# Optimization experiments

Measured on AMD Instinct MI355X. Metric: run time of the kernel, lower is better.

## Reference

```python
import math
import jax, jax.numpy as jnp
import numpy as np

N_HEAD = 16
N_EMBD = 1024
HEAD_DIM = N_EMBD // N_HEAD  # 64
SHARED = 16
PRIV = HEAD_DIM - SHARED     # 48
B, T = 4, 2048
STD = 0.02


def setup_inputs() -> dict:
    key = jax.random.key(0)
    ks = jax.random.split(key, 6)
    x = jax.random.normal(ks[0], (B, T, N_EMBD), dtype=jnp.float32)
    # Linear params stored as (in, out); bias zeros per _reset_parameters
    W_share = jax.random.normal(ks[1], (N_EMBD, SHARED), dtype=jnp.float32) * STD
    Wq = jax.random.normal(ks[2], (N_EMBD, N_HEAD * PRIV), dtype=jnp.float32) * STD
    Wk = jax.random.normal(ks[3], (N_EMBD, N_HEAD * PRIV), dtype=jnp.float32) * STD
    Wv = jax.random.normal(ks[4], (N_EMBD, N_EMBD), dtype=jnp.float32) * STD
    Wo = jax.random.normal(ks[5], (N_EMBD, N_EMBD), dtype=jnp.float32) * STD
    return {
        'hidden_states': x,
        'W_share': W_share, 'b_share': jnp.zeros((SHARED,), jnp.float32),
        'Wq': Wq, 'bq': jnp.zeros((N_HEAD * PRIV,), jnp.float32),
        'Wk': Wk, 'bk': jnp.zeros((N_HEAD * PRIV,), jnp.float32),
        'Wv': Wv, 'bv': jnp.zeros((N_EMBD,), jnp.float32),
        'Wo': Wo, 'bo': jnp.zeros((N_EMBD,), jnp.float32),
    }


def reference(hidden_states, W_share, b_share, Wq, bq, Wk, bk, Wv, bv, Wo, bo):
    x = hidden_states
    Bt, Tt, C = x.shape
    # shared projection, broadcast across heads: (B,T,s) -> (B,H,T,s)
    share = x @ W_share + b_share
    share_h = jnp.broadcast_to(share[:, None, :, :], (Bt, N_HEAD, Tt, SHARED))
    # private q/k: (B,T,H*p) -> (B,H,T,p)
    q_priv = (x @ Wq + bq).reshape(Bt, Tt, N_HEAD, PRIV).transpose(0, 2, 1, 3)
    k_priv = (x @ Wk + bk).reshape(Bt, Tt, N_HEAD, PRIV).transpose(0, 2, 1, 3)
    q = jnp.concatenate([share_h, q_priv], axis=-1)  # (B,H,T,head_dim)
    k = jnp.concatenate([share_h, k_priv], axis=-1)
    v = (x @ Wv + bv).reshape(Bt, Tt, N_HEAD, HEAD_DIM).transpose(0, 2, 1, 3)
    scale = 1.0 / math.sqrt(HEAD_DIM)
    att = jnp.einsum('bhqd,bhkd->bhqk', q, k) * scale
    causal = jnp.tril(jnp.ones((Tt, Tt), dtype=bool))
    att = jnp.where(causal[None, None, :, :], att, -jnp.inf)
    att = jax.nn.softmax(att, axis=-1)
    y = jnp.einsum('bhqk,bhkd->bhqd', att, v)
    y = y.transpose(0, 2, 1, 3).reshape(Bt, Tt, C)
    y = y @ Wo + bo
    return y
```

## Files before the change

kernel.cpp:

```cpp
#include <hip/hip_runtime.h>
#include <hip/hip_bf16.h>

typedef unsigned short u16;
typedef short short8 __attribute__((ext_vector_type(8)));
typedef float f32x4 __attribute__((ext_vector_type(4)));

#define N_EMBD   1024
#define N_HEADS  16
#define HEAD_DIM 64
#define PRIV     48
#define SEQ_T    2048
#define BATCH    4
#define M_ROWS   (BATCH*SEQ_T)
#define PNS      2816
#define NTILES   (SEQ_T/64)
#define NT_K     16

#if __has_builtin(__builtin_amdgcn_exp2f)
#define EXP2(x) __builtin_amdgcn_exp2f(x)
#else
#define EXP2(x) exp2f(x)
#endif

#if __has_builtin(__builtin_amdgcn_global_load_lds)
#define HAVE_GLL 1
#else
#define HAVE_GLL 0
#endif

__device__ __forceinline__ u16 f2bf(float f) {
  __hip_bfloat16 h = __float2bfloat16(f);
  return *reinterpret_cast<u16*>(&h);
}
__device__ __forceinline__ float bf2f(u16 s) {
  __hip_bfloat16 h;
  *reinterpret_cast<u16*>(&h) = s;
  return __bfloat162float(h);
}
__device__ __forceinline__ float loadv(const void* p, size_t i, int isf32) {
  return isf32 ? ((const float*)p)[i] : bf2f(((const u16*)p)[i]);
}
__device__ __forceinline__ u16 truncbf(float f) {
  unsigned u = __builtin_bit_cast(unsigned, f);
  return (u16)(u >> 16);
}
#if HAVE_GLL
__device__ __forceinline__ void gload_lds16(const u16* g, u16* l) {
  __builtin_amdgcn_global_load_lds(
      (const __attribute__((address_space(1))) void*)g,
      (__attribute__((address_space(3))) void*)l, 16, 0, 0);
}
#endif

__global__ __launch_bounds__(256) void detect_kernel(const u16* __restrict__ x,
                                                     int* __restrict__ flag) {
  __shared__ int cnt;
  if (threadIdx.x == 0) cnt = 0;
  __syncthreads();
  u16 v = x[2 * threadIdx.x];
  int e = (v >> 7) & 0xFF;
  int junk = (e >= 0xC0 || (e != 0 && e <= 0x30)) ? 1 : 0;
  if (junk) atomicAdd(&cnt, 1);
  __syncthreads();
  if (threadIdx.x == 0) *flag = (cnt > 16) ? 1 : 0;
}

__global__ __launch_bounds__(256) void pack_t_kernel(
    const void* __restrict__ Wsh, const void* __restrict__ Wq,
    const void* __restrict__ Wk,  const void* __restrict__ Wv,
    const void* __restrict__ Wo,
    const void* __restrict__ bsh, const void* __restrict__ bq,
    const void* __restrict__ bk,  const void* __restrict__ bv,
    const void* __restrict__ bo,
    u16* __restrict__ Wcat, u16* __restrict__ Woc,
    u16* __restrict__ bcat, u16* __restrict__ boc,
    const int* __restrict__ flagp)
{
  const int f = *flagp;
  if (blockIdx.z == 5) {
    const int flat = blockIdx.y * 16 + blockIdx.x;
    const int padN = (PNS - 2576) * 1024;
    for (int i = flat * 256 + threadIdx.x; i < padN; i += 256 * 256)
      Wcat[(size_t)2576 * 1024 + i] = 0;
    if (flat == 0) {
      for (int c = threadIdx.x; c < PNS; c += 256) {
        float v = 0.f;
        if (c < 16)        v = loadv(bsh, c, f);
        else if (c < 784)  v = loadv(bq, c - 16, f);
        else if (c < 1552) v = loadv(bk, c - 784, f);
        else if (c < 2576) v = loadv(bv, c - 1552, f);
        bcat[c] = f2bf(v);
      }
    } else if (flat == 1) {
      for (int c = threadIdx.x; c < N_EMBD; c += 256)
        boc[c] = f2bf(loadv(bo, c, f));
    }
    return;
  }
  const void* src; u16* dst; int N, rowOff;
  switch (blockIdx.z) {
    case 0: src = Wsh; dst = Wcat; N = 16;   rowOff = 0;    break;
    case 1: src = Wq;  dst = Wcat; N = 768;  rowOff = 16;   break;
    case 2: src = Wk;  dst = Wcat; N = 768;  rowOff = 784;  break;
    case 3: src = Wv;  dst = Wcat; N = 1024; rowOff = 1552; break;
    default:src = Wo;  dst = Woc;  N = 1024; rowOff = 0;    break;
  }
  const int n0 = blockIdx.x * 64;
  if (n0 >= N) return;
  const int k0 = blockIdx.y * 64;
  __shared__ u16 t[64][65];
  const int tx = threadIdx.x & 63, ty = threadIdx.x >> 6;
#pragma unroll
  for (int rr = 0; rr < 16; rr++) {
    int k = k0 + ty * 16 + rr;
    int n = n0 + tx;
    float v = (n < N) ? loadv(src, (size_t)k * N + n, f) : 0.f;
    t[ty * 16 + rr][tx] = f2bf(v);
  }
  __syncthreads();
#pragma unroll
  for (int rr = 0; rr < 16; rr++) {
    int n = ty * 16 + rr;
    if (n0 + n < N)
      dst[(size_t)(rowOff + n0 + n) * 1024 + k0 + tx] = t[tx][n];
  }
}

__global__ __launch_bounds__(256) void xbf_kernel(const void* __restrict__ x,
                                                  u16* __restrict__ Xb,
                                                  const int* __restrict__ flagp) {
  const int f = *flagp;
  const size_t i = (size_t)blockIdx.x * 256 + threadIdx.x;
  if (f) {
    const float4* p = (const float4*)x;
    float4 a = p[i * 2], b = p[i * 2 + 1];
    u16 t[8] = {f2bf(a.x), f2bf(a.y), f2bf(a.z), f2bf(a.w),
                f2bf(b.x), f2bf(b.y), f2bf(b.z), f2bf(b.w)};
    *(uint4*)&Xb[i * 8] = *(const uint4*)t;
  } else {
    *(uint4*)&Xb[i * 8] = ((const uint4*)x)[i];
  }
}

__global__ __launch_bounds__(512, 2) void gemm8p_kernel(
    const u16* __restrict__ A,
    const u16* __restrict__ Bt,
    const u16* __restrict__ bias,
    void* __restrict__ C, int ldc, int Mtiles,
    const int* __restrict__ flagp, int c_dyn)
{
  __shared__ __align__(16) u16 smem[73728];
  u16* const As = smem;
  u16* const Bs = smem + 3 * 8192;

  const bool cf32 = (c_dyn != 0) && (*flagp != 0);

  const int tid  = threadIdx.x;
  const int lane = tid & 63;
  const int w    = tid >> 6;
  const int quad = lane >> 4, l16 = lane & 15;
  const int wm   = w >> 2, wn = w & 3;

  const int nwg = gridDim.x;
  const int wg  = (blockIdx.x & 7) * (nwg >> 3) + (blockIdx.x >> 3);
  const int mb  = wg % Mtiles, nb = wg / Mtiles;
  const int m0  = mb * 128, n0 = nb * 256;

  int ldsA[2]; size_t glA[2];
  int ldsB[2][2]; size_t glB[2][2];
#pragma unroll
  for (int rd = 0; rd < 2; rd++) {
    int j = tid + rd * 512, rp = j >> 3, s = j & 7;
    int cl = (s ^ (rp & 7)) * 8;
    ldsA[rd] = rp * 64 + s * 8;
    glA[rd]  = (size_t)(m0 + rp) * 1024 + cl;
#pragma unroll
    for (int nh = 0; nh < 2; nh++) {
      int cc = (rp & 31) + nh * 32 + (rp >> 5) * 64;
      ldsB[nh][rd] = cc * 64 + s * 8;
      glB[nh][rd]  = (size_t)(n0 + cc) * 1024 + cl;
    }
  }

#if HAVE_GLL
#define G8(g, l) gload_lds16((g), (l))
#else
#define G8(g, l) (*(uint4*)(l) = *(const uint4*)(g))
#endif
#define STG_A(t, bf)                                                       \
  if ((t) < NT_K) {                                                        \
    _Pragma("unroll") for (int rd = 0; rd < 2; rd++)                       \
      G8(A + glA[rd] + (t) * 64, As + (bf) * 8192 + ldsA[rd]);             \
  }
#define STG_B(nh, t, bf)                                                   \
  if ((t) < NT_K) {                                                        \
    _Pragma("unroll") for (int rd = 0; rd < 2; rd++)                       \
      G8(Bt + glB[nh][rd] + (t) * 64, Bs + (bf) * 16384 + ldsB[nh][rd]);   \
  }

  const int ck0  = ((quad)     ^ (l16 & 7)) * 8;
  const int ck1  = ((4 + quad) ^ (l16 & 7)) * 8;
  const int arow = (wm * 64 + l16) * 64;
  const int brow = (wn * 64 + l16) * 64;

  f32x4 acc[4][4];
#pragma unroll
  for (int i = 0; i < 4; i++)
#pragma unroll
    for (int j = 0; j < 4; j++) acc[i][j] = (f32x4){0.f, 0.f, 0.f, 0.f};

  short8 af[4][2], bA[2][2], bB[2][2];

#define READ_A(cur)                                                        \
  { const u16* pa = As + (cur) * 8192 + arow;                              \
    _Pragma("unroll") for (int m = 0; m < 4; m++) {                        \
      af[m][0] = *(const short8*)(pa + m * 1024 + ck0);                    \
      af[m][1] = *(const short8*)(pa + m * 1024 + ck1); } }
#define READ_B(dst, nh, cur)                                               \
  { const u16* pb = Bs + (cur) * 16384 + brow + (nh) * 2048;               \
    _Pragma("unroll") for (int n = 0; n < 2; n++) {                        \
      dst[n][0] = *(const short8*)(pb + n * 1024 + ck0);                   \
      dst[n][1] = *(const short8*)(pb + n * 1024 + ck1); } }
#define MM16(bfr, nh)                                                      \
  __builtin_amdgcn_s_setprio(1);                                           \
  _Pragma("unroll") for (int m = 0; m < 4; m++)                            \
    _Pragma("unroll") for (int n = 0; n < 2; n++) {                        \
      acc[m][(nh)*2+n] = __builtin_amdgcn_mfma_f32_16x16x32_bf16(          \
          af[m][0], bfr[n][0], acc[m][(nh)*2+n], 0, 0, 0);                 \
      acc[m][(nh)*2+n] = __builtin_amdgcn_mfma_f32_16x16x32_bf16(          \
          af[m][1], bfr[n][1], acc[m][(nh)*2+n], 0, 0, 0); }               \
  __builtin_amdgcn_s_setprio(0);
#define BARR { __builtin_amdgcn_s_barrier(); __builtin_amdgcn_sched_barrier(0); }

  STG_A(0, 0); STG_B(1, 0, 0); STG_B(0, 0, 0);
  STG_A(1, 1); STG_B(1, 1, 1); STG_B(0, 1, 1);
  asm volatile("s_waitcnt vmcnt(6)");
  BARR;

#pragma unroll
  for (int kt = 0; kt < NT_K; kt++) {
    const int cur = kt % 3;
    const int stb = (kt + 2) % 3;
    READ_A(cur); READ_B(bA, 0, cur);
    STG_A(kt + 2, stb); STG_B(1, kt + 2, stb);
    BARR;
    MM16(bA, 0);
    BARR;
    READ_B(bB, 1, cur);
    STG_B(0, kt + 2, stb);
    BARR;
    MM16(bB, 1);
    if (kt < NT_K - 2)       { asm volatile("s_waitcnt vmcnt(6)"); }
    else if (kt == NT_K - 2) { asm volatile("s_waitcnt vmcnt(0)"); }
    BARR;
  }
#undef STG_A
#undef STG_B
#undef READ_A
#undef READ_B
#undef MM16
#undef BARR
#undef G8

  float bvv[4];
#pragma unroll
  for (int ni = 0; ni < 4; ni++)
    bvv[ni] = bf2f(bias[n0 + wn * 64 + ni * 16 + l16]);

  if (!cf32) {
    u16* cs = smem + w * 4096;
#pragma unroll
    for (int m = 0; m < 4; m++)
#pragma unroll
      for (int ni = 0; ni < 4; ni++)
#pragma unroll
        for (int r = 0; r < 4; r++) {
          int row = m * 16 + quad * 4 + r;
          int ch  = ((ni * 2 + (l16 >> 3)) ^ (row & 7)) * 8 + (l16 & 7);
          cs[row * 64 + ch] = f2bf(acc[m][ni][r] + bvv[ni]);
        }
    u16* Cb = (u16*)C;
#pragma unroll
    for (int i = 0; i < 8; i++) {
      int ch = lane + i * 64;
      int rr = ch >> 3, cc = ch & 7;
      short8 v = *(const short8*)(cs + rr * 64 + ((cc ^ (rr & 7)) * 8));
      *(short8*)&Cb[(size_t)(m0 + wm * 64 + rr) * ldc + n0 + wn * 64 + cc * 8] = v;
    }
  } else {
    float* cf = (float*)(void*)smem + w * 2048;
#pragma unroll
    for (int pass = 0; pass < 2; pass++) {
#pragma unroll
      for (int m2 = 0; m2 < 2; m2++)
#pragma unroll
        for (int ni = 0; ni < 4; ni++)
#pragma unroll
          for (int r = 0; r < 4; r++) {
            int row = m2 * 16 + quad * 4 + r;
            int ch  = ((ni * 4 + (l16 >> 2)) ^ (row & 15)) * 4 + (l16 & 3);
            cf[row * 64 + ch] = acc[pass * 2 + m2][ni][r] + bvv[ni];
          }
      float* Cf = (float*)C;
#pragma unroll
      for (int i = 0; i < 8; i++) {
        int ch = lane + i * 64;
        int rr = ch >> 4, cc = ch & 15;
        f32x4 v = *(const f32x4*)(cf + rr * 64 + ((cc ^ (rr & 15)) * 4));
        *(f32x4*)&Cf[(size_t)(m0 + wm * 64 + pass * 32 + rr) * ldc +
                     n0 + wn * 64 + cc * 4] = v;
      }
    }
  }
}

__global__ __launch_bounds__(256) void vt_kernel(const u16* __restrict__ P,
                                                 u16* __restrict__ Vt)
{
  const int tt = blockIdx.x * 64;
  const int bh = blockIdx.y;
  const int b = bh >> 4, h = bh & 15;
  const int vcol = 1552 + h * HEAD_DIM;
  __shared__ u16 t[64][65];
  const int tx = threadIdx.x & 63, ty = threadIdx.x >> 6;
#pragma unroll
  for (int rr = 0; rr < 16; rr++) {
    int r = ty * 16 + rr;
    t[r][tx] = P[((size_t)b * SEQ_T + tt + r) * PNS + vcol + tx];
  }
  __syncthreads();
#pragma unroll
  for (int rr = 0; rr < 16; rr++) {
    int d = ty * 16 + rr;
    Vt[((size_t)bh * 64 + d) * SEQ_T + tt + tx] = t[tx][d];
  }
}

__global__ __launch_bounds__(256, 2) void attn_kernel(
    const u16* __restrict__ P, const u16* __restrict__ Vt,
    u16* __restrict__ Y)
{
  const int bh  = blockIdx.x;
  const int b   = bh >> 4, h = bh & 15;
  const int p   = blockIdx.y;
  const int qtA = p, qtB = NTILES - 1 - p;
  const int tid = threadIdx.x;
  const int w   = tid >> 6;
  const int lane = tid & 63;
  const int quad = lane >> 4, l16 = lane & 15;
  const size_t rowb = (size_t)b * SEQ_T;
  const int qcol = 16 + h * PRIV;
  const int kcol = 784 + h * PRIV;

  __shared__ __align__(16) u16 Ks[3][64 * 64];
  __shared__ __align__(16) u16 Vs[3][64 * 64];
  __shared__ __align__(16) u16 Ps[4][2][16 * 68];

  const float csc = 0.18033688011112042f;
  const int d0  = quad * 8;
  const int cq0 = (d0 < 16) ? d0 : (qcol + d0 - 16);
  const int iA = qtA * 64 + w * 16, iB = qtB * 64 + w * 16;
  const u16* qrowA = P + (rowb + iA + l16) * PNS;
  const u16* qrowB = P + (rowb + iB + l16) * PNS;
  short8 qaA0 = *(const short8*)&qrowA[cq0];
  short8 qaA1 = *(const short8*)&qrowA[qcol + 16 + d0];
  short8 qaB0 = *(const short8*)&qrowB[cq0];
  short8 qaB1 = *(const short8*)&qrowB[qcol + 16 + d0];
#pragma unroll
  for (int e = 0; e < 8; e++) {
    qaA0[e] = (short)f2bf(bf2f((u16)qaA0[e]) * csc);
    qaA1[e] = (short)f2bf(bf2f((u16)qaA1[e]) * csc);
    qaB0[e] = (short)f2bf(bf2f((u16)qaB0[e]) * csc);
    qaB1[e] = (short)f2bf(bf2f((u16)qaB1[e]) * csc);
  }
  short8 ones;
#pragma unroll
  for (int e = 0; e < 8; e++) ones[e] = (short)0x3F80;

  const int nkt = qtB + 1;

#if HAVE_GLL
#define GLOADA(g, l) gload_lds16((g), (l))
#else
#define GLOADA(g, l) (*(uint4*)(l) = *(const uint4*)(g))
#endif
#define STAGE_KV(t, bb)                                                        \
  {                                                                            \
    const int kk0 = (t) * 64;                                                  \
    _Pragma("unroll") for (int i2 = 0; i2 < 2; i2++) {                         \
      int c   = tid + i2 * 256;                                                \
      int row = c >> 3;                                                        \
      int dg  = ((c & 7) ^ (row & 7)) * 8;                                     \
      int col = (dg < 16) ? dg : (kcol + dg - 16);                             \
      GLOADA(&P[(rowb + kk0 + row) * PNS + col], &Ks[bb][c * 8]);              \
      GLOADA(&Vt[((size_t)bh * 64 + row) * SEQ_T + kk0 + dg], &Vs[bb][c * 8]); \
    }                                                                          \
  }

  f32x4 accyA[4], accyB[4], acclA, acclB;
#pragma unroll
  for (int g = 0; g < 4; g++) {
    accyA[g] = (f32x4){0.f, 0.f, 0.f, 0.f};
    accyB[g] = (f32x4){0.f, 0.f, 0.f, 0.f};
  }
  acclA = (f32x4){0.f, 0.f, 0.f, 0.f};
  acclB = (f32x4){0.f, 0.f, 0.f, 0.f};

  STAGE_KV(0, 0);
  STAGE_KV(1, 1);
  asm volatile("s_waitcnt vmcnt(4)" ::: "memory");
  __builtin_amdgcn_sched_barrier(0);
  __builtin_amdgcn_s_barrier();

  for (int kt = 0; kt < nkt; kt++) {
    const int cur = kt % 3;
    const int k0  = kt * 64;
    if (kt + 2 < nkt) STAGE_KV(kt + 2, (kt + 2) % 3);

    const bool doA = (kt <= qtA);

    float svA[4][4], svB[4][4];
    __builtin_amdgcn_s_setprio(1);
#pragma unroll
    for (int g = 0; g < 4; g++) {
      int j = g * 16 + l16;
      short8 kb0 = *(const short8*)&Ks[cur][j * 64 + ((quad    ) ^ (j & 7)) * 8];
      short8 kb1 = *(const short8*)&Ks[cur][j * 64 + ((quad + 4) ^ (j & 7)) * 8];
      f32x4 sB = (f32x4){0.f, 0.f, 0.f, 0.f};
      sB = __builtin_amdgcn_mfma_f32_16x16x32_bf16(qaB0, kb0, sB, 0, 0, 0);
      sB = __builtin_amdgcn_mfma_f32_16x16x32_bf16(qaB1, kb1, sB, 0, 0, 0);
#pragma unroll
      for (int r = 0; r < 4; r++) svB[g][r] = sB[r];
      if (doA) {
        f32x4 sA = (f32x4){0.f, 0.f, 0.f, 0.f};
        sA = __builtin_amdgcn_mfma_f32_16x16x32_bf16(qaA0, kb0, sA, 0, 0, 0);
        sA = __builtin_amdgcn_mfma_f32_16x16x32_bf16(qaA1, kb1, sA, 0, 0, 0);
#pragma unroll
        for (int r = 0; r < 4; r++) svA[g][r] = sA[r];
      }
    }
    __builtin_amdgcn_s_setprio(0);
    if (kt == qtA && doA) {
#pragma unroll
      for (int g = 0; g < 4; g++)
#pragma unroll
        for (int r = 0; r < 4; r++) {
          int gi = iA + quad * 4 + r;
          int gj = k0 + g * 16 + l16;
          if (gj > gi) svA[g][r] = -__builtin_inff();
        }
    }
    if (kt == qtB) {
#pragma unroll
      for (int g = 0; g < 4; g++)
#pragma unroll
        for (int r = 0; r < 4; r++) {
          int gi = iB + quad * 4 + r;
          int gj = k0 + g * 16 + l16;
          if (gj > gi) svB[g][r] = -__builtin_inff();
        }
    }

    if (doA) {
#pragma unroll
      for (int g = 0; g < 4; g++)
#pragma unroll
        for (int r = 0; r < 4; r++)
          Ps[w][0][(quad * 4 + r) * 68 + g * 16 + l16] = truncbf(EXP2(svA[g][r]));
    }
#pragma unroll
    for (int g = 0; g < 4; g++)
#pragma unroll
      for (int r = 0; r < 4; r++)
        Ps[w][1][(quad * 4 + r) * 68 + g * 16 + l16] = truncbf(EXP2(svB[g][r]));

    __builtin_amdgcn_s_setprio(1);
#pragma unroll
    for (int kf = 0; kf < 2; kf++) {
      short8 vb[4];
#pragma unroll
      for (int g2 = 0; g2 < 4; g2++) {
        int row = g2 * 16 + l16;
        vb[g2] = *(const short8*)&Vs[cur][row * 64 + (((kf * 4 + quad) ^ (row & 7)) * 8)];
      }
      short8 paB = *(const short8*)&Ps[w][1][l16 * 68 + kf * 32 + quad * 8];
      acclB = __builtin_amdgcn_mfma_f32_16x16x32_bf16(paB, ones, acclB, 0, 0, 0);
#pragma unroll
      for (int g2 = 0; g2 < 4; g2++)
        accyB[g2] = __builtin_amdgcn_mfma_f32_16x16x32_bf16(paB, vb[g2], accyB[g2], 0, 0, 0);
      if (doA) {
        short8 paA = *(const short8*)&Ps[w][0][l16 * 68 + kf * 32 + quad * 8];
        acclA = __builtin_amdgcn_mfma_f32_16x16x32_bf16(paA, ones, acclA, 0, 0, 0);
#pragma unroll
        for (int g2 = 0; g2 < 4; g2++)
          accyA[g2] = __builtin_amdgcn_mfma_f32_16x16x32_bf16(paA, vb[g2], accyA[g2], 0, 0, 0);
      }
    }
    __builtin_amdgcn_s_setprio(0);

    if (kt + 3 < nkt) {
      asm volatile("s_waitcnt vmcnt(4)" ::: "memory");
      __builtin_amdgcn_sched_barrier(0);
      __builtin_amdgcn_s_barrier();
    } else if (kt + 2 == nkt) {
      asm volatile("s_waitcnt vmcnt(0)" ::: "memory");
      __builtin_amdgcn_sched_barrier(0);
      __builtin_amdgcn_s_barrier();
    } else if (kt + 3 == nkt) {
      asm volatile("s_waitcnt vmcnt(4)" ::: "memory");
      __builtin_amdgcn_sched_barrier(0);
      __builtin_amdgcn_s_barrier();
    }
  }
#undef STAGE_KV
#undef GLOADA

  float invA[4], invB[4];
#pragma unroll
  for (int r = 0; r < 4; r++) {
    invA[r] = 1.0f / acclA[r];
    invB[r] = 1.0f / acclB[r];
  }
#pragma unroll
  for (int g2 = 0; g2 < 4; g2++) {
    int col = h * HEAD_DIM + g2 * 16 + l16;
#pragma unroll
    for (int r = 0; r < 4; r++) {
      int giA = iA + quad * 4 + r;
      int giB = iB + quad * 4 + r;
      Y[(rowb + giA) * N_EMBD + col] = f2bf(accyA[g2][r] * invA[r]);
      Y[(rowb + giB) * N_EMBD + col] = f2bf(accyB[g2][r] * invB[r]);
    }
  }
}

extern "C" void kernel_launch(void* const* d_in, const int* in_sizes, int n_in,
                              void* d_out, int out_size, void* d_ws, size_t ws_size,
                              hipStream_t stream) {
  (void)in_sizes; (void)n_in; (void)out_size; (void)ws_size;
  const void* x   = d_in[0];
  const void* Wsh = d_in[1];
  const void* bsh = d_in[2];
  const void* Wq  = d_in[3];
  const void* bq  = d_in[4];
  const void* Wk  = d_in[5];
  const void* bk  = d_in[6];
  const void* Wv  = d_in[7];
  const void* bv  = d_in[8];
  const void* Wo  = d_in[9];
  const void* bo  = d_in[10];

  char* wsb = (char*)d_ws;
  int* flag = (int*)wsb;
  u16* ws16 = (u16*)(wsb + 64);
  u16* Wcat = ws16;
  u16* bcat = Wcat + (size_t)PNS * N_EMBD;
  u16* Woc  = bcat + PNS;
  u16* boc  = Woc + (size_t)N_EMBD * N_EMBD;
  u16* Pb   = boc + N_EMBD;
  u16* Yb   = Pb + (size_t)M_ROWS * PNS;
  u16* Vtb  = Yb + (size_t)M_ROWS * N_EMBD;
  u16* Xb   = Yb;

  detect_kernel<<<dim3(1), dim3(256), 0, stream>>>((const u16*)x, flag);
  pack_t_kernel<<<dim3(16, 16, 6), dim3(256), 0, stream>>>(
      Wsh, Wq, Wk, Wv, Wo, bsh, bq, bk, bv, bo, Wcat, Woc, bcat, boc, flag);
  xbf_kernel<<<dim3(M_ROWS * N_EMBD / (256 * 8)), dim3(256), 0, stream>>>(
      x, Xb, flag);
  gemm8p_kernel<<<dim3(64 * (PNS / 256)), dim3(512), 0, stream>>>(
      Xb, Wcat, bcat, Pb, PNS, 64, flag, 0);
  vt_kernel<<<dim3(SEQ_T / 64, BATCH * N_HEADS), dim3(256), 0, stream>>>(
      Pb, Vtb);
  attn_kernel<<<dim3(BATCH * N_HEADS, NTILES / 2), dim3(256), 0, stream>>>(
      Pb, Vtb, Yb);
  gemm8p_kernel<<<dim3(64 * (N_EMBD / 256)), dim3(512), 0, stream>>>(
      Yb, Woc, boc, d_out, N_EMBD, 64, flag, 1);
}
```

Baseline: 284.0 us.

## Switch attention to 32x32 MFMA with register-resident P via lane shuffles

Rewrites the attention inner loop to use 32x32x16 MFMA tiles that cover both the A and B query blocks in one 32-row tile, computing S transposed so that P stays in registers. P is packed to bf16 with v_cvt_pk and exchanged across half-waves with shuffles instead of going through LDS. The per-warp P shared buffer is removed and launch bounds are raised to 3 blocks per CU. The tradeoff is that A rows are computed even when masked (kt > qtA), which wastes MFMA work on those blocks, and the change adds shuffle cost and register pressure.

```diff
diff --git a/kernel.cpp b/kernel.cpp
--- a/kernel.cpp
+++ b/kernel.cpp
@@ -4,6 +4,8 @@
 typedef unsigned short u16;
 typedef short short8 __attribute__((ext_vector_type(8)));
 typedef float f32x4 __attribute__((ext_vector_type(4)));
+typedef float f32x16 __attribute__((ext_vector_type(16)));
+typedef unsigned uint32x4 __attribute__((ext_vector_type(4)));
 
 #define N_EMBD   1024
 #define N_HEADS  16
@@ -336,7 +338,7 @@
   }
 }
 
-__global__ __launch_bounds__(256, 2) void attn_kernel(
+__global__ __launch_bounds__(256, 3) void attn_kernel(
     const u16* __restrict__ P, const u16* __restrict__ Vt,
     u16* __restrict__ Y)
 {
@@ -347,32 +349,30 @@
   const int tid = threadIdx.x;
   const int w   = tid >> 6;
   const int lane = tid & 63;
-  const int quad = lane >> 4, l16 = lane & 15;
+  const int l32 = lane & 31, hi = lane >> 5;
   const size_t rowb = (size_t)b * SEQ_T;
   const int qcol = 16 + h * PRIV;
   const int kcol = 784 + h * PRIV;
 
   __shared__ __align__(16) u16 Ks[3][64 * 64];
   __shared__ __align__(16) u16 Vs[3][64 * 64];
-  __shared__ __align__(16) u16 Ps[4][2][16 * 68];
 
   const float csc = 0.18033688011112042f;
-  const int d0  = quad * 8;
-  const int cq0 = (d0 < 16) ? d0 : (qcol + d0 - 16);
   const int iA = qtA * 64 + w * 16, iB = qtB * 64 + w * 16;
-  const u16* qrowA = P + (rowb + iA + l16) * PNS;
-  const u16* qrowB = P + (rowb + iB + l16) * PNS;
-  short8 qaA0 = *(const short8*)&qrowA[cq0];
-  short8 qaA1 = *(const short8*)&qrowA[qcol + 16 + d0];
-  short8 qaB0 = *(const short8*)&qrowB[cq0];
-  short8 qaB1 = *(const short8*)&qrowB[qcol + 16 + d0];
-#pragma unroll
-  for (int e = 0; e < 8; e++) {
-    qaA0[e] = (short)f2bf(bf2f((u16)qaA0[e]) * csc);
-    qaA1[e] = (short)f2bf(bf2f((u16)qaA1[e]) * csc);
-    qaB0[e] = (short)f2bf(bf2f((u16)qaB0[e]) * csc);
-    qaB1[e] = (short)f2bf(bf2f((u16)qaB1[e]) * csc);
-  }
+  const int gi = (l32 < 16) ? (iA + l32) : (iB + l32 - 16);
+  const u16* qptr = P + (rowb + gi) * PNS;
+
+  short8 qb[4];
+  qb[0] = *(const short8*)&qptr[8 * hi];
+#pragma unroll
+  for (int c = 1; c < 4; c++)
+    qb[c] = *(const short8*)&qptr[qcol + 16 * c + 8 * hi - 16];
+#pragma unroll
+  for (int c = 0; c < 4; c++)
+#pragma unroll
+    for (int e = 0; e < 8; e++)
+      qb[c][e] = (short)f2bf(bf2f((u16)qb[c][e]) * csc);
+
   short8 ones;
 #pragma unroll
   for (int e = 0; e < 8; e++) ones[e] = (short)0x3F80;
@@ -397,14 +397,11 @@
     }                                                                          \
   }
 
-  f32x4 accyA[4], accyB[4], acclA, acclB;
-#pragma unroll
-  for (int g = 0; g < 4; g++) {
-    accyA[g] = (f32x4){0.f, 0.f, 0.f, 0.f};
-    accyB[g] = (f32x4){0.f, 0.f, 0.f, 0.f};
-  }
-  acclA = (f32x4){0.f, 0.f, 0.f, 0.f};
-  acclB = (f32x4){0.f, 0.f, 0.f, 0.f};
+  f32x16 accy[2], accl;
+#pragma unroll
+  for (int r = 0; r < 16; r++) { accy[0][r] = 0.f; accy[1][r] = 0.f; accl[r] = 0.f; }
+
+  const float ninf = -__builtin_inff();
 
   STAGE_KV(0, 0);
   STAGE_KV(1, 1);
@@ -417,86 +414,66 @@
     const int k0  = kt * 64;
     if (kt + 2 < nkt) STAGE_KV(kt + 2, (kt + 2) % 3);
 
-    const bool doA = (kt <= qtA);
-
-    float svA[4][4], svB[4][4];
-    __builtin_amdgcn_s_setprio(1);
-#pragma unroll
-    for (int g = 0; g < 4; g++) {
-      int j = g * 16 + l16;
-      short8 kb0 = *(const short8*)&Ks[cur][j * 64 + ((quad    ) ^ (j & 7)) * 8];
-      short8 kb1 = *(const short8*)&Ks[cur][j * 64 + ((quad + 4) ^ (j & 7)) * 8];
-      f32x4 sB = (f32x4){0.f, 0.f, 0.f, 0.f};
-      sB = __builtin_amdgcn_mfma_f32_16x16x32_bf16(qaB0, kb0, sB, 0, 0, 0);
-      sB = __builtin_amdgcn_mfma_f32_16x16x32_bf16(qaB1, kb1, sB, 0, 0, 0);
-#pragma unroll
-      for (int r = 0; r < 4; r++) svB[g][r] = sB[r];
-      if (doA) {
-        f32x4 sA = (f32x4){0.f, 0.f, 0.f, 0.f};
-        sA = __builtin_amdgcn_mfma_f32_16x16x32_bf16(qaA0, kb0, sA, 0, 0, 0);
-        sA = __builtin_amdgcn_mfma_f32_16x16x32_bf16(qaA1, kb1, sA, 0, 0, 0);
-#pragma unroll
-        for (int r = 0; r < 4; r++) svA[g][r] = sA[r];
+#pragma unroll
+    for (int kk = 0; kk < 2; kk++) {
+      f32x16 s;
+#pragma unroll
+      for (int r = 0; r < 16; r++) s[r] = 0.f;
+      const int krow = kk * 32 + l32;
+      __builtin_amdgcn_s_setprio(1);
+#pragma unroll
+      for (int c = 0; c < 4; c++) {
+        short8 ka = *(const short8*)&Ks[cur][krow * 64 + (((2 * c + hi) ^ (krow & 7)) * 8)];
+        s = __builtin_amdgcn_mfma_f32_32x32x16_bf16(ka, qb[c], s, 0, 0, 0);
+      }
+      __builtin_amdgcn_s_setprio(0);
+
+      if (kt == qtA || kt == qtB) {
+#pragma unroll
+        for (int r = 0; r < 16; r++) {
+          int gj = k0 + kk * 32 + (r & 3) + 8 * (r >> 2) + 4 * hi;
+          if (gj > gi) s[r] = ninf;
+        }
+      }
+      if (kt > qtA) {
+#pragma unroll
+        for (int r = 0; r < 16; r++)
+          if (l32 < 16) s[r] = ninf;
+      }
+
+      float px[16];
+#pragma unroll
+      for (int r = 0; r < 16; r++) px[r] = EXP2(s[r]);
+
+#pragma unroll
+      for (int kc = 0; kc < 2; kc++) {
+        unsigned g0, g1, g2, g3;
+        asm("v_cvt_pk_bf16_f32 %0, %1, %2" : "=v"(g0) : "v"(px[8*kc+0]), "v"(px[8*kc+1]));
+        asm("v_cvt_pk_bf16_f32 %0, %1, %2" : "=v"(g1) : "v"(px[8*kc+2]), "v"(px[8*kc+3]));
+        asm("v_cvt_pk_bf16_f32 %0, %1, %2" : "=v"(g2) : "v"(px[8*kc+4]), "v"(px[8*kc+5]));
+        asm("v_cvt_pk_bf16_f32 %0, %1, %2" : "=v"(g3) : "v"(px[8*kc+6]), "v"(px[8*kc+7]));
+        unsigned x0 = (unsigned)__shfl_xor((int)g0, 32);
+        unsigned x1 = (unsigned)__shfl_xor((int)g1, 32);
+        unsigned x2 = (unsigned)__shfl_xor((int)g2, 32);
+        unsigned x3 = (unsigned)__shfl_xor((int)g3, 32);
+        unsigned v0 = hi ? x2 : g0;
+        unsigned v1 = hi ? x3 : g1;
+        unsigned v2 = hi ? g2 : x0;
+        unsigned v3 = hi ? g3 : x1;
+        uint32x4 pv = {v0, v1, v2, v3};
+        short8 pa = __builtin_bit_cast(short8, pv);
+
+        __builtin_amdgcn_s_setprio(1);
+        accl = __builtin_amdgcn_mfma_f32_32x32x16_bf16(pa, ones, accl, 0, 0, 0);
+#pragma unroll
+        for (int dt = 0; dt < 2; dt++) {
+          int vrow = dt * 32 + l32;
+          short8 vbf = *(const short8*)&Vs[cur][vrow * 64 + (((4*kk + 2*kc + hi) ^ (vrow & 7)) * 8)];
+          accy[dt] = __builtin_amdgcn_mfma_f32_32x32x16_bf16(pa, vbf, accy[dt], 0, 0, 0);
+        }
+        __builtin_amdgcn_s_setprio(0);
       }
     }
-    __builtin_amdgcn_s_setprio(0);
-    if (kt == qtA && doA) {
-#pragma unroll
-      for (int g = 0; g < 4; g++)
-#pragma unroll
-        for (int r = 0; r < 4; r++) {
-          int gi = iA + quad * 4 + r;
-          int gj = k0 + g * 16 + l16;
-          if (gj > gi) svA[g][r] = -__builtin_inff();
-        }
-    }
-    if (kt == qtB) {
-#pragma unroll
-      for (int g = 0; g < 4; g++)
-#pragma unroll
-        for (int r = 0; r < 4; r++) {
-          int gi = iB + quad * 4 + r;
-          int gj = k0 + g * 16 + l16;
-          if (gj > gi) svB[g][r] = -__builtin_inff();
-        }
-    }
-
-    if (doA) {
-#pragma unroll
-      for (int g = 0; g < 4; g++)
-#pragma unroll
-        for (int r = 0; r < 4; r++)
-          Ps[w][0][(quad * 4 + r) * 68 + g * 16 + l16] = truncbf(EXP2(svA[g][r]));
-    }
-#pragma unroll
-    for (int g = 0; g < 4; g++)
-#pragma unroll
-      for (int r = 0; r < 4; r++)
-        Ps[w][1][(quad * 4 + r) * 68 + g * 16 + l16] = truncbf(EXP2(svB[g][r]));
-
-    __builtin_amdgcn_s_setprio(1);
-#pragma unroll
-    for (int kf = 0; kf < 2; kf++) {
-      short8 vb[4];
-#pragma unroll
-      for (int g2 = 0; g2 < 4; g2++) {
-        int row = g2 * 16 + l16;
-        vb[g2] = *(const short8*)&Vs[cur][row * 64 + (((kf * 4 + quad) ^ (row & 7)) * 8)];
-      }
-      short8 paB = *(const short8*)&Ps[w][1][l16 * 68 + kf * 32 + quad * 8];
-      acclB = __builtin_amdgcn_mfma_f32_16x16x32_bf16(paB, ones, acclB, 0, 0, 0);
-#pragma unroll
-      for (int g2 = 0; g2 < 4; g2++)
-        accyB[g2] = __builtin_amdgcn_mfma_f32_16x16x32_bf16(paB, vb[g2], accyB[g2], 0, 0, 0);
-      if (doA) {
-        short8 paA = *(const short8*)&Ps[w][0][l16 * 68 + kf * 32 + quad * 8];
-        acclA = __builtin_amdgcn_mfma_f32_16x16x32_bf16(paA, ones, acclA, 0, 0, 0);
-#pragma unroll
-        for (int g2 = 0; g2 < 4; g2++)
-          accyA[g2] = __builtin_amdgcn_mfma_f32_16x16x32_bf16(paA, vb[g2], accyA[g2], 0, 0, 0);
-      }
-    }
-    __builtin_amdgcn_s_setprio(0);
 
     if (kt + 3 < nkt) {
       asm volatile("s_waitcnt vmcnt(4)" ::: "memory");
@@ -515,22 +492,16 @@
 #undef STAGE_KV
 #undef GLOADA
 
-  float invA[4], invB[4];
-#pragma unroll
-  for (int r = 0; r < 4; r++) {
-    invA[r] = 1.0f / acclA[r];
-    invB[r] = 1.0f / acclB[r];
-  }
-#pragma unroll
-  for (int g2 = 0; g2 < 4; g2++) {
-    int col = h * HEAD_DIM + g2 * 16 + l16;
-#pragma unroll
-    for (int r = 0; r < 4; r++) {
-      int giA = iA + quad * 4 + r;
-      int giB = iB + quad * 4 + r;
-      Y[(rowb + giA) * N_EMBD + col] = f2bf(accyA[g2][r] * invA[r]);
-      Y[(rowb + giB) * N_EMBD + col] = f2bf(accyB[g2][r] * invB[r]);
-    }
+  float inv[16];
+#pragma unroll
+  for (int r = 0; r < 16; r++) inv[r] = 1.0f / accl[r];
+#pragma unroll
+  for (int r = 0; r < 16; r++) {
+    int q = (r & 3) + 8 * (r >> 2) + 4 * hi;
+    int grow = (r < 8) ? (iA + q) : (iB + q - 16);
+    size_t base = (rowb + grow) * N_EMBD + h * HEAD_DIM + l32;
+    Y[base]      = f2bf(accy[0][r] * inv[r]);
+    Y[base + 32] = f2bf(accy[1][r] * inv[r]);
   }
 }
 
```

Measured after the change: 300.5 us. +5.8%, slower.
